# Optimization experiments

Hardware: AMD Instinct MI355X
Metric: run time of the kernel (lower is better)

The kernel has to match this reference:

```python
import jax, jax.numpy as jnp
import numpy as np

N, D, DB, E, H = 1024, 512, 64, 32768, 1024

def setup_inputs() -> dict:
    key = jax.random.key(0)
    k = jax.random.split(key, 6)
    object_feats = jax.random.normal(k[0], (N, D), dtype=jnp.float32)
    bboxes_embedding = jax.random.normal(k[1], (N, N, DB), dtype=jnp.float32)
    pairs = jax.random.randint(k[2], (E, 2), 0, N, dtype=jnp.int64)
    # Kaiming-normal-ish init for the two Linear layers
    W1 = jax.random.normal(k[3], (D + D + DB, H), dtype=jnp.float32) * np.sqrt(2.0 / (D + D + DB))
    b1 = jnp.zeros((H,), dtype=jnp.float32)
    W2 = jax.random.normal(k[4], (H, D), dtype=jnp.float32) * np.sqrt(2.0 / H)
    b2 = jnp.zeros((D,), dtype=jnp.float32)
    return {"object_feats": object_feats, "bboxes_embedding": bboxes_embedding,
            "pairs": pairs, "W1": W1, "b1": b1, "W2": W2, "b2": b2}

def reference(object_feats, bboxes_embedding, pairs, W1, b1, W2, b2):
    sub = pairs[:, 0]
    obj = pairs[:, 1]
    # gather pair features: [E, D] each, plus pairwise bbox embedding [E, DB]
    f_sub = object_feats[sub]
    f_obj = object_feats[obj]
    bb = bboxes_embedding[sub, obj]
    x = jnp.concatenate((f_sub, f_obj, bb), axis=1)  # [E, 2D+DB]
    h = jax.nn.relu(x @ W1 + b1)
    out = h @ W2 + b2  # [E, D]
    n = object_feats.shape[0]
    # scatter-mean into subject nodes; each node's own feature is included once,
    # so new_feat[i] = (object_feats[i] + sum_{pairs with sub==i} out) / (1 + count[i]).
    # Nodes with no incident pairs keep their original feature (count==0 -> identity).
    seg_sum = jax.ops.segment_sum(out, sub, num_segments=n)  # [N, D]
    count = jax.ops.segment_sum(jnp.ones((out.shape[0],), dtype=out.dtype), sub, num_segments=n)
    new_feats = (object_feats + seg_sum) / (1.0 + count)[:, None]
    return (new_feats, bboxes_embedding, pairs)
```

## Files before the change

### kernel.cpp

```cpp
#include <hip/hip_runtime.h>

#define N_OBJ 1024
#define E_P   32768

typedef float f32x4 __attribute__((ext_vector_type(4)));
typedef short bf16x8 __attribute__((ext_vector_type(8)));
typedef unsigned short u16x4 __attribute__((ext_vector_type(4)));

__device__ __forceinline__ unsigned short f2bf(float f) {
    unsigned u = __float_as_uint(f);
    u = u + 0x7FFFu + ((u >> 16) & 1u);
    return (unsigned short)(u >> 16);
}

#define CP_OFF_PREP 0
#define CP_LEN_PREP 2097152
#define CP_OFF_PRE  (CP_OFF_PREP + CP_LEN_PREP)
#define CP_LEN_PRE  1048576
#define CP_OFF_PQ   (CP_OFF_PRE + CP_LEN_PRE)
#define CP_LEN_PQ   3145728
#define CP_OFF_SEG  (CP_OFF_PQ + CP_LEN_PQ)
#define CP_LEN_SEG  5242880
#define CP_OFF_OUT  (CP_OFF_SEG + CP_LEN_SEG)
#define CP_LEN_OUT  5242880

__device__ __forceinline__ void copy_role(const float4* __restrict__ src,
                                          float4* __restrict__ dst,
                                          int off, int len, int nblocks, int cb) {
    int i = off + cb * 256 + threadIdx.x;
    int end = off + len;
    int stride = nblocks * 256;
    for (; i < end; i += stride) dst[i] = src[i];
}

__global__ __launch_bounds__(256) void k_prep(const float* __restrict__ W1,
                                              const float* __restrict__ W2,
                                              const float* __restrict__ feats,
                                              unsigned short* __restrict__ w1pqT,
                                              unsigned short* __restrict__ w1cT,
                                              unsigned short* __restrict__ w2T,
                                              unsigned short* __restrict__ featsb,
                                              const float4* __restrict__ csrc,
                                              float4* __restrict__ cdst) {
    int bid = blockIdx.x;
    if ((bid % 3) == 2) { copy_role(csrc, cdst, CP_OFF_PREP, CP_LEN_PREP, 928, bid / 3); return; }
    int job = (bid / 3) * 2 + (bid % 3);
    int tid = threadIdx.x;
    if (job >= 1600) {
        int base = (job - 1600) * 2048 + tid * 8;
        float4 v0 = *(const float4*)&feats[base];
        float4 v1 = *(const float4*)&feats[base + 4];
        u16x4 o0 = { f2bf(v0.x), f2bf(v0.y), f2bf(v0.z), f2bf(v0.w) };
        u16x4 o1 = { f2bf(v1.x), f2bf(v1.y), f2bf(v1.z), f2bf(v1.w) };
        *(u16x4*)&featsb[base] = o0;
        *(u16x4*)&featsb[base + 4] = o1;
        return;
    }
    const float* in; unsigned short* out;
    int LDI, LDO, r0, c0, nbase, kbase;
    if (job < 1024) {
        int t = job; r0 = (t >> 5) * 32; c0 = (t & 31) * 32;
        in = W1; LDI = 1024; out = w1pqT; LDO = 512;
        nbase = c0 + (r0 >= 512 ? 1024 : 0); kbase = r0 & 511;
    } else if (job < 1088) {
        int t = job - 1024; r0 = 1024 + (t >> 5) * 32; c0 = (t & 31) * 32;
        in = W1; LDI = 1024; out = w1cT; LDO = 64;
        nbase = c0; kbase = r0 - 1024;
    } else {
        int t = job - 1088; r0 = (t >> 4) * 32; c0 = (t & 15) * 32;
        in = W2; LDI = 512; out = w2T; LDO = 1024;
        nbase = c0; kbase = r0;
    }
    __shared__ float lds[32][33];
    int ti = tid >> 3, tj = (tid & 7) * 4;
    float4 v = *(const float4*)&in[(size_t)(r0 + ti) * LDI + c0 + tj];
    lds[ti][tj] = v.x; lds[ti][tj + 1] = v.y; lds[ti][tj + 2] = v.z; lds[ti][tj + 3] = v.w;
    __syncthreads();
    int oc = tid >> 3, oj = (tid & 7) * 4;
    u16x4 o = { f2bf(lds[oj][oc]), f2bf(lds[oj + 1][oc]), f2bf(lds[oj + 2][oc]), f2bf(lds[oj + 3][oc]) };
    *(u16x4*)&out[(size_t)(nbase + oc) * LDO + kbase + oj] = o;
}

__global__ __launch_bounds__(256) void k_pre(const int* __restrict__ pairs,
                                             float* __restrict__ out_pairs,
                                             int* __restrict__ counts,
                                             const float4* __restrict__ csrc,
                                             float4* __restrict__ cdst) {
    int bid = blockIdx.x;
    if ((bid % 3) < 2) { copy_role(csrc, cdst, CP_OFF_PRE, CP_LEN_PRE, 512, (bid / 3) * 2 + (bid % 3)); return; }
    int i = (bid / 3) * 256 + threadIdx.x;
    if (i < 2 * E_P) out_pairs[i] = (float)pairs[i];
    if (i < E_P) atomicAdd(&counts[pairs[2 * i]], 1);
}

__global__ __launch_bounds__(256) void k_scan(const int* __restrict__ counts,
                                              int* __restrict__ offsets,
                                              int* __restrict__ cursor,
                                              int* __restrict__ brec,
                                              int* __restrict__ bcnt) {
    __shared__ int buf[2][256];
    int tid = threadIdx.x;
    int c[4]; int s = 0;
    #pragma unroll
    for (int i = 0; i < 4; ++i) { c[i] = counts[tid * 4 + i]; s += c[i]; }
    buf[0][tid] = s;
    __syncthreads();
    int sel = 0;
    for (int d = 1; d < 256; d <<= 1) {
        int v = buf[sel][tid];
        if (tid >= d) v += buf[sel][tid - d];
        buf[sel ^ 1][tid] = v;
        sel ^= 1;
        __syncthreads();
    }
    int base = buf[sel][tid] - s;
    int run = base;
    #pragma unroll
    for (int i = 0; i < 4; ++i) {
        offsets[tid * 4 + i] = run;
        cursor[tid * 4 + i]  = run;
        run += c[i];
    }
    if (tid == 255) offsets[1024] = run;
    int nb[4]; int t = 0;
    #pragma unroll
    for (int i = 0; i < 4; ++i) { nb[i] = (c[i] + 15) >> 4; t += nb[i]; }
    __syncthreads();
    buf[0][tid] = t;
    __syncthreads();
    sel = 0;
    for (int d = 1; d < 256; d <<= 1) {
        int v = buf[sel][tid];
        if (tid >= d) v += buf[sel][tid - d];
        buf[sel ^ 1][tid] = v;
        sel ^= 1;
        __syncthreads();
    }
    int bpos = buf[sel][tid] - t;
    #pragma unroll
    for (int i = 0; i < 4; ++i) {
        int seg = tid * 4 + i;
        for (int k = 0; k < nb[i]; ++k) brec[bpos++] = (seg << 8) | k;
    }
    if (tid == 255) bcnt[0] = bpos;
}

__global__ __launch_bounds__(256) void k_pq(const unsigned short* __restrict__ featsb,
                                            const unsigned short* __restrict__ w1pqT,
                                            const float* __restrict__ b1,
                                            float* __restrict__ P, float* __restrict__ Q,
                                            const int* __restrict__ pairs,
                                            int* __restrict__ cursor,
                                            int* __restrict__ csr,
                                            const float4* __restrict__ csrc,
                                            float4* __restrict__ cdst) {
    int bid = blockIdx.x;
    if (bid >= 1536) {
        int e = (bid - 1536) * 256 + threadIdx.x;
        if (e < E_P) {
            int sidx = pairs[2 * e];
            int pos = atomicAdd(&cursor[sidx], 1);
            csr[pos] = e;
        }
        return;
    }
    if ((bid % 3) < 2) { copy_role(csrc, cdst, CP_OFF_PQ, CP_LEN_PQ, 1024, (bid / 3) * 2 + (bid % 3)); return; }
    int job = bid / 3;
    int m0 = (job >> 5) * 64, n0 = (job & 31) * 64;
    int tid = threadIdx.x, w = tid >> 6, l = tid & 63;
    int ln = l & 15, kb = (l >> 4) * 8;
    int row = m0 + w * 16 + ln;
    f32x4 acc[4] = {};
    for (int k0 = 0; k0 < 512; k0 += 32) {
        bf16x8 a = *(const bf16x8*)&featsb[(size_t)row * 512 + k0 + kb];
        #pragma unroll
        for (int f = 0; f < 4; ++f) {
            bf16x8 b = *(const bf16x8*)&w1pqT[(size_t)(n0 + f * 16 + ln) * 512 + k0 + kb];
            acc[f] = __builtin_amdgcn_mfma_f32_16x16x32_bf16(a, b, acc[f], 0, 0, 0);
        }
    }
    int mr = m0 + w * 16 + (l >> 4) * 4;
    if (n0 < 1024) {
        #pragma unroll
        for (int f = 0; f < 4; ++f) {
            int n = n0 + f * 16 + ln;
            float b1v = b1[n];
            #pragma unroll
            for (int r = 0; r < 4; ++r)
                P[(size_t)(mr + r) * 1024 + n] = acc[f][r] + b1v;
        }
    } else {
        #pragma unroll
        for (int f = 0; f < 4; ++f) {
            int n = n0 - 1024 + f * 16 + ln;
            #pragma unroll
            for (int r = 0; r < 4; ++r)
                Q[(size_t)(mr + r) * 1024 + n] = acc[f][r];
        }
    }
}

__global__ __launch_bounds__(256) void k_seg(const int* __restrict__ csr,
                                             const int* __restrict__ offsets,
                                             const int* __restrict__ brec,
                                             const int* __restrict__ bcnt,
                                             const int* __restrict__ pairs,
                                             const float* __restrict__ bb,
                                             const unsigned short* __restrict__ w1cT,
                                             const float* __restrict__ P,
                                             const float* __restrict__ Q,
                                             float* __restrict__ HS,
                                             const float4* __restrict__ csrc,
                                             float4* __restrict__ cdst) {
    int bid = blockIdx.x;
    if ((bid % 3) == 0) { copy_role(csrc, cdst, CP_OFF_SEG, CP_LEN_SEG, 1536, bid / 3); return; }
    int b = (bid / 3) * 2 + (bid % 3) - 1;
    if (b >= bcnt[0]) return;
    int rec = brec[b];
    int seg = rec >> 8, kchunk = rec & 255;
    int start = offsets[seg] + kchunk * 16;
    int end = offsets[seg + 1];
    int n = end - start; if (n > 16) n = 16;

    const int tid = threadIdx.x, w = tid >> 6, l = tid & 63;
    const int ln = l & 15, g = l >> 4, kb = g * 8;
    const int n0 = w * 256;

    int idx = start + ln; int last = end - 1; if (idx > last) idx = last;
    int e = csr[idx];
    int obj = pairs[2 * e + 1];
    const float* br = &bb[((size_t)seg * 1024 + (size_t)obj) * 64];
    float4 a0 = *(const float4*)&br[kb];
    float4 a1 = *(const float4*)&br[kb + 4];
    float4 a2 = *(const float4*)&br[32 + kb];
    float4 a3 = *(const float4*)&br[32 + kb + 4];
    bf16x8 A0, A1;
    A0[0] = (short)f2bf(a0.x); A0[1] = (short)f2bf(a0.y); A0[2] = (short)f2bf(a0.z); A0[3] = (short)f2bf(a0.w);
    A0[4] = (short)f2bf(a1.x); A0[5] = (short)f2bf(a1.y); A0[6] = (short)f2bf(a1.z); A0[7] = (short)f2bf(a1.w);
    A1[0] = (short)f2bf(a2.x); A1[1] = (short)f2bf(a2.y); A1[2] = (short)f2bf(a2.z); A1[3] = (short)f2bf(a2.w);
    A1[4] = (short)f2bf(a3.x); A1[5] = (short)f2bf(a3.y); A1[6] = (short)f2bf(a3.z); A1[7] = (short)f2bf(a3.w);

    int ra0 = __shfl(obj, g * 4 + 0);
    int ra1 = __shfl(obj, g * 4 + 1);
    int ra2 = __shfl(obj, g * 4 + 2);
    int ra3 = __shfl(obj, g * 4 + 3);
    bool v0 = (g * 4 + 0) < n;
    bool v1 = (g * 4 + 1) < n;
    bool v2 = (g * 4 + 2) < n;
    bool v3 = (g * 4 + 3) < n;

    float pv[16];
    #pragma unroll
    for (int f = 0; f < 16; ++f)
        pv[f] = P[(size_t)seg * 1024 + n0 + f * 16 + ln];

    #pragma unroll
    for (int f = 0; f < 16; ++f) {
        const unsigned short* wr = &w1cT[(size_t)(n0 + f * 16 + ln) * 64];
        bf16x8 b0 = *(const bf16x8*)&wr[kb];
        bf16x8 b1v = *(const bf16x8*)&wr[32 + kb];
        f32x4 d = {0.f, 0.f, 0.f, 0.f};
        d = __builtin_amdgcn_mfma_f32_16x16x32_bf16(A0, b0, d, 0, 0, 0);
        d = __builtin_amdgcn_mfma_f32_16x16x32_bf16(A1, b1v, d, 0, 0, 0);
        int col = n0 + f * 16 + ln;
        float q0 = Q[(size_t)ra0 * 1024 + col];
        float q1 = Q[(size_t)ra1 * 1024 + col];
        float q2 = Q[(size_t)ra2 * 1024 + col];
        float q3 = Q[(size_t)ra3 * 1024 + col];
        float h = 0.f;
        h += v0 ? fmaxf(d[0] + pv[f] + q0, 0.f) : 0.f;
        h += v1 ? fmaxf(d[1] + pv[f] + q1, 0.f) : 0.f;
        h += v2 ? fmaxf(d[2] + pv[f] + q2, 0.f) : 0.f;
        h += v3 ? fmaxf(d[3] + pv[f] + q3, 0.f) : 0.f;
        h += __shfl_xor(h, 16);
        h += __shfl_xor(h, 32);
        if (l < 16) atomicAdd(&HS[(size_t)seg * 1024 + n0 + f * 16 + l], h);
    }
}

__global__ __launch_bounds__(256) void k_out(const float* __restrict__ HS,
                                             const unsigned short* __restrict__ w2T,
                                             const float* __restrict__ feats,
                                             const float* __restrict__ b2,
                                             const int* __restrict__ counts,
                                             float* __restrict__ out0,
                                             const float4* __restrict__ csrc,
                                             float4* __restrict__ cdst) {
    int bid = blockIdx.x;
    if ((bid % 13) != 12) { copy_role(csrc, cdst, CP_OFF_OUT, CP_LEN_OUT, 1536, (bid / 13) * 12 + (bid % 13)); return; }
    int job = bid / 13;
    int m0 = (job >> 3) * 64, n0 = (job & 7) * 64;
    int tid = threadIdx.x, w = tid >> 6, l = tid & 63;
    int ln = l & 15, kb = (l >> 4) * 8;
    int row = m0 + w * 16 + ln;
    f32x4 acc[4] = {};
    for (int k0 = 0; k0 < 1024; k0 += 32) {
        const float* hp = &HS[(size_t)row * 1024 + k0 + kb];
        float4 h0 = *(const float4*)&hp[0];
        float4 h1 = *(const float4*)&hp[4];
        bf16x8 a;
        a[0] = (short)f2bf(h0.x); a[1] = (short)f2bf(h0.y); a[2] = (short)f2bf(h0.z); a[3] = (short)f2bf(h0.w);
        a[4] = (short)f2bf(h1.x); a[5] = (short)f2bf(h1.y); a[6] = (short)f2bf(h1.z); a[7] = (short)f2bf(h1.w);
        #pragma unroll
        for (int f = 0; f < 4; ++f) {
            bf16x8 b = *(const bf16x8*)&w2T[(size_t)(n0 + f * 16 + ln) * 1024 + k0 + kb];
            acc[f] = __builtin_amdgcn_mfma_f32_16x16x32_bf16(a, b, acc[f], 0, 0, 0);
        }
    }
    int mr = m0 + w * 16 + (l >> 4) * 4;
    float cv[4], inv[4];
    #pragma unroll
    for (int r = 0; r < 4; ++r) {
        float c = (float)counts[mr + r];
        cv[r] = c;
        inv[r] = 1.0f / (1.0f + c);
    }
    #pragma unroll
    for (int f = 0; f < 4; ++f) {
        int n = n0 + f * 16 + ln;
        float b2v = b2[n];
        #pragma unroll
        for (int r = 0; r < 4; ++r) {
            float fv = feats[(size_t)(mr + r) * 512 + n];
            out0[(size_t)(mr + r) * 512 + n] = (fv + acc[f][r] + cv[r] * b2v) * inv[r];
        }
    }
}

extern "C" void kernel_launch(void* const* d_in, const int* in_sizes, int n_in,
                              void* d_out, int out_size, void* d_ws, size_t ws_size,
                              hipStream_t stream) {
    const float* feats = (const float*)d_in[0];
    const float* bb    = (const float*)d_in[1];
    const int*   pairs = (const int*)d_in[2];
    const float* W1    = (const float*)d_in[3];
    const float* b1    = (const float*)d_in[4];
    const float* W2    = (const float*)d_in[5];
    const float* b2    = (const float*)d_in[6];

    float* out        = (float*)d_out;
    float* out_feats  = out;
    float* out_bb     = out + (size_t)N_OBJ * 512;
    float* out_pairs  = out + (size_t)N_OBJ * 512 + (size_t)N_OBJ * N_OBJ * 64;

    char* w = (char*)d_ws;
    unsigned short* featsb = (unsigned short*)w;
    unsigned short* w1pqT  = (unsigned short*)(w + (1u << 20));
    float*          HS     = (float*)w;
    unsigned short* w1cT   = (unsigned short*)(w + (4u << 20));
    unsigned short* w2T    = (unsigned short*)(w + (4u << 20) + (128u << 10));
    float* P = (float*)(w + (5u << 20) + (128u << 10));
    float* Q = (float*)(w + (9u << 20) + (128u << 10));
    char* ints = w + (13u << 20) + (128u << 10);
    int* counts  = (int*)ints;
    int* offsets = (int*)(ints + 4096);
    int* cursor  = (int*)(ints + 12288);
    int* csr     = (int*)(ints + 16384);
    int* brec    = (int*)(ints + 16384 + 131072);
    int* bcnt    = (int*)(ints + 16384 + 131072 + 16384);

    const float4* cbb  = (const float4*)bb;
    float4*       cobb = (float4*)out_bb;

    hipMemsetAsync(counts, 0, 4096, stream);

    k_prep<<<2784, 256, 0, stream>>>(W1, W2, feats, w1pqT, w1cT, w2T, featsb, cbb, cobb);
    k_pre<<<768, 256, 0, stream>>>(pairs, out_pairs, counts, cbb, cobb);
    k_scan<<<1, 256, 0, stream>>>(counts, offsets, cursor, brec, bcnt);
    k_pq<<<1664, 256, 0, stream>>>(featsb, w1pqT, b1, P, Q, pairs, cursor, csr, cbb, cobb);

    hipMemsetAsync(HS, 0, (size_t)N_OBJ * 1024 * sizeof(float), stream);

    k_seg<<<4608, 256, 0, stream>>>(csr, offsets, brec, bcnt, pairs, bb, w1cT, P, Q, HS, cbb, cobb);
    k_out<<<1664, 256, 0, stream>>>(HS, w2T, feats, b2, counts, out_feats, cbb, cobb);
}
```

Baseline: 248.1 us.

## Merge prep kernels, pack CSR records, process 32 pairs per segment block

Merges k_prep and k_pre into one kernel, and gives the scan kernel extra blocks that do part of the bbox copy. The CSR now stores object indices directly, and block records pack start, segment and count, so k_seg avoids the offsets and pairs lookups. Each k_seg block now handles up to 32 pairs as two MFMA groups that share the weight loads and the HS atomics, which halves the number of atomics and blocks. The copy work is rebalanced across kernels and the copy loop is unrolled by two, at the cost of higher register pressure in k_seg.

```diff
diff --git a/kernel.cpp b/kernel.cpp
--- a/kernel.cpp
+++ b/kernel.cpp
@@ -13,39 +13,53 @@
     return (unsigned short)(u >> 16);
 }
 
-#define CP_OFF_PREP 0
-#define CP_LEN_PREP 2097152
-#define CP_OFF_PRE  (CP_OFF_PREP + CP_LEN_PREP)
-#define CP_LEN_PRE  1048576
-#define CP_OFF_PQ   (CP_OFF_PRE + CP_LEN_PRE)
-#define CP_LEN_PQ   3145728
-#define CP_OFF_SEG  (CP_OFF_PQ + CP_LEN_PQ)
-#define CP_LEN_SEG  5242880
-#define CP_OFF_OUT  (CP_OFF_SEG + CP_LEN_SEG)
-#define CP_LEN_OUT  5242880
+#define OFF_A    0
+#define LEN_A    2097152
+#define OFF_SCAN (OFF_A + LEN_A)
+#define LEN_SCAN 1048576
+#define OFF_PQ   (OFF_SCAN + LEN_SCAN)
+#define LEN_PQ   3145728
+#define OFF_SEG  (OFF_PQ + LEN_PQ)
+#define LEN_SEG  7340032
+#define OFF_OUT  (OFF_SEG + LEN_SEG)
+#define LEN_OUT  3145728
 
 __device__ __forceinline__ void copy_role(const float4* __restrict__ src,
                                           float4* __restrict__ dst,
-                                          int off, int len, int nblocks, int cb) {
+                                          int off, int len, int nb, int cb) {
+    int stride = nb * 256;
     int i = off + cb * 256 + threadIdx.x;
     int end = off + len;
-    int stride = nblocks * 256;
-    for (; i < end; i += stride) dst[i] = src[i];
-}
-
-__global__ __launch_bounds__(256) void k_prep(const float* __restrict__ W1,
-                                              const float* __restrict__ W2,
-                                              const float* __restrict__ feats,
-                                              unsigned short* __restrict__ w1pqT,
-                                              unsigned short* __restrict__ w1cT,
-                                              unsigned short* __restrict__ w2T,
-                                              unsigned short* __restrict__ featsb,
-                                              const float4* __restrict__ csrc,
-                                              float4* __restrict__ cdst) {
-    int bid = blockIdx.x;
-    if ((bid % 3) == 2) { copy_role(csrc, cdst, CP_OFF_PREP, CP_LEN_PREP, 928, bid / 3); return; }
+    for (; i + stride < end; i += 2 * stride) {
+        float4 a = src[i];
+        float4 b = src[i + stride];
+        dst[i] = a;
+        dst[i + stride] = b;
+    }
+    if (i < end) dst[i] = src[i];
+}
+
+__global__ __launch_bounds__(256) void k_a(const float* __restrict__ W1,
+                                           const float* __restrict__ W2,
+                                           const float* __restrict__ feats,
+                                           const int* __restrict__ pairs,
+                                           unsigned short* __restrict__ w1pqT,
+                                           unsigned short* __restrict__ w1cT,
+                                           unsigned short* __restrict__ w2T,
+                                           unsigned short* __restrict__ featsb,
+                                           float* __restrict__ out_pairs,
+                                           int* __restrict__ counts,
+                                           const float4* __restrict__ csrc,
+                                           float4* __restrict__ cdst) {
+    int bid = blockIdx.x, tid = threadIdx.x;
+    if ((bid % 3) == 2) { copy_role(csrc, cdst, OFF_A, LEN_A, 1056, bid / 3); return; }
     int job = (bid / 3) * 2 + (bid % 3);
-    int tid = threadIdx.x;
+    if (job >= 1856) {
+        int i = (job - 1856) * 256 + tid;
+        out_pairs[i] = (float)pairs[i];
+        if (i < E_P) atomicAdd(&counts[pairs[2 * i]], 1);
+        return;
+    }
     if (job >= 1600) {
         int base = (job - 1600) * 2048 + tid * 8;
         float4 v0 = *(const float4*)&feats[base];
@@ -59,7 +73,7 @@
     const float* in; unsigned short* out;
     int LDI, LDO, r0, c0, nbase, kbase;
     if (job < 1024) {
-        int t = job; r0 = (t >> 5) * 32; c0 = (t & 31) * 32;
+        r0 = (job >> 5) * 32; c0 = (job & 31) * 32;
         in = W1; LDI = 1024; out = w1pqT; LDO = 512;
         nbase = c0 + (r0 >= 512 ? 1024 : 0); kbase = r0 & 511;
     } else if (job < 1088) {
@@ -77,29 +91,20 @@
     lds[ti][tj] = v.x; lds[ti][tj + 1] = v.y; lds[ti][tj + 2] = v.z; lds[ti][tj + 3] = v.w;
     __syncthreads();
     int oc = tid >> 3, oj = (tid & 7) * 4;
-    u16x4 o = { f2bf(lds[oj][oc]), f2bf(lds[oj + 1][oc]), f2bf(lds[oj + 2][oc]), f2bf(lds[oj + 3][oc]) };
+    u16x4 o = { f2bf(lds[oj][oc]), f2bf(lds[oj + 1][oc]),
+                f2bf(lds[oj + 2][oc]), f2bf(lds[oj + 3][oc]) };
     *(u16x4*)&out[(size_t)(nbase + oc) * LDO + kbase + oj] = o;
 }
 
-__global__ __launch_bounds__(256) void k_pre(const int* __restrict__ pairs,
-                                             float* __restrict__ out_pairs,
-                                             int* __restrict__ counts,
-                                             const float4* __restrict__ csrc,
-                                             float4* __restrict__ cdst) {
-    int bid = blockIdx.x;
-    if ((bid % 3) < 2) { copy_role(csrc, cdst, CP_OFF_PRE, CP_LEN_PRE, 512, (bid / 3) * 2 + (bid % 3)); return; }
-    int i = (bid / 3) * 256 + threadIdx.x;
-    if (i < 2 * E_P) out_pairs[i] = (float)pairs[i];
-    if (i < E_P) atomicAdd(&counts[pairs[2 * i]], 1);
-}
-
 __global__ __launch_bounds__(256) void k_scan(const int* __restrict__ counts,
-                                              int* __restrict__ offsets,
                                               int* __restrict__ cursor,
-                                              int* __restrict__ brec,
-                                              int* __restrict__ bcnt) {
+                                              unsigned* __restrict__ brec,
+                                              int* __restrict__ bcnt,
+                                              const float4* __restrict__ csrc,
+                                              float4* __restrict__ cdst) {
+    int bid = blockIdx.x, tid = threadIdx.x;
+    if (bid != 0) { copy_role(csrc, cdst, OFF_SCAN, LEN_SCAN, 1024, bid - 1); return; }
     __shared__ int buf[2][256];
-    int tid = threadIdx.x;
     int c[4]; int s = 0;
     #pragma unroll
     for (int i = 0; i < 4; ++i) { c[i] = counts[tid * 4 + i]; s += c[i]; }
@@ -116,15 +121,10 @@
     int base = buf[sel][tid] - s;
     int run = base;
     #pragma unroll
-    for (int i = 0; i < 4; ++i) {
-        offsets[tid * 4 + i] = run;
-        cursor[tid * 4 + i]  = run;
-        run += c[i];
-    }
-    if (tid == 255) offsets[1024] = run;
+    for (int i = 0; i < 4; ++i) { cursor[tid * 4 + i] = run; run += c[i]; }
     int nb[4]; int t = 0;
     #pragma unroll
-    for (int i = 0; i < 4; ++i) { nb[i] = (c[i] + 15) >> 4; t += nb[i]; }
+    for (int i = 0; i < 4; ++i) { nb[i] = (c[i] + 31) >> 5; t += nb[i]; }
     __syncthreads();
     buf[0][tid] = t;
     __syncthreads();
@@ -137,10 +137,16 @@
         __syncthreads();
     }
     int bpos = buf[sel][tid] - t;
+    int run2 = base;
     #pragma unroll
     for (int i = 0; i < 4; ++i) {
         int seg = tid * 4 + i;
-        for (int k = 0; k < nb[i]; ++k) brec[bpos++] = (seg << 8) | k;
+        for (int k = 0; k < nb[i]; ++k) {
+            int st = run2 + k * 32;
+            int cnt = c[i] - k * 32; if (cnt > 32) cnt = 32;
+            brec[bpos++] = (unsigned)st | ((unsigned)seg << 16) | ((unsigned)(cnt - 1) << 26);
+        }
+        run2 += c[i];
     }
     if (tid == 255) bcnt[0] = bpos;
 }
@@ -151,20 +157,18 @@
                                             float* __restrict__ P, float* __restrict__ Q,
                                             const int* __restrict__ pairs,
                                             int* __restrict__ cursor,
-                                            int* __restrict__ csr,
+                                            int* __restrict__ csr_obj,
                                             const float4* __restrict__ csrc,
                                             float4* __restrict__ cdst) {
     int bid = blockIdx.x;
     if (bid >= 1536) {
         int e = (bid - 1536) * 256 + threadIdx.x;
-        if (e < E_P) {
-            int sidx = pairs[2 * e];
-            int pos = atomicAdd(&cursor[sidx], 1);
-            csr[pos] = e;
-        }
+        int sidx = pairs[2 * e];
+        int pos = atomicAdd(&cursor[sidx], 1);
+        csr_obj[pos] = pairs[2 * e + 1];
         return;
     }
-    if ((bid % 3) < 2) { copy_role(csrc, cdst, CP_OFF_PQ, CP_LEN_PQ, 1024, (bid / 3) * 2 + (bid % 3)); return; }
+    if ((bid % 3) < 2) { copy_role(csrc, cdst, OFF_PQ, LEN_PQ, 1024, (bid / 3) * 2 + (bid % 3)); return; }
     int job = bid / 3;
     int m0 = (job >> 5) * 64, n0 = (job & 31) * 64;
     int tid = threadIdx.x, w = tid >> 6, l = tid & 63;
@@ -200,11 +204,9 @@
     }
 }
 
-__global__ __launch_bounds__(256) void k_seg(const int* __restrict__ csr,
-                                             const int* __restrict__ offsets,
-                                             const int* __restrict__ brec,
+__global__ __launch_bounds__(256) void k_seg(const int* __restrict__ csr_obj,
+                                             const unsigned* __restrict__ brec,
                                              const int* __restrict__ bcnt,
-                                             const int* __restrict__ pairs,
                                              const float* __restrict__ bb,
                                              const unsigned short* __restrict__ w1cT,
                                              const float* __restrict__ P,
@@ -213,65 +215,84 @@
                                              const float4* __restrict__ csrc,
                                              float4* __restrict__ cdst) {
     int bid = blockIdx.x;
-    if ((bid % 3) == 0) { copy_role(csrc, cdst, CP_OFF_SEG, CP_LEN_SEG, 1536, bid / 3); return; }
-    int b = (bid / 3) * 2 + (bid % 3) - 1;
+    if ((bid % 2) == 0) { copy_role(csrc, cdst, OFF_SEG, LEN_SEG, 2048, bid / 2); return; }
+    int b = bid / 2;
     if (b >= bcnt[0]) return;
-    int rec = brec[b];
-    int seg = rec >> 8, kchunk = rec & 255;
-    int start = offsets[seg] + kchunk * 16;
-    int end = offsets[seg + 1];
-    int n = end - start; if (n > 16) n = 16;
+    unsigned rec = brec[b];
+    const int start = rec & 0xFFFF;
+    const int seg = (rec >> 16) & 0x3FF;
+    const int n = ((rec >> 26) & 31) + 1;
 
     const int tid = threadIdx.x, w = tid >> 6, l = tid & 63;
-    const int ln = l & 15, g = l >> 4, kb = g * 8;
+    const int ln = l & 15, g4 = l >> 4, kb = g4 * 8;
     const int n0 = w * 256;
-
-    int idx = start + ln; int last = end - 1; if (idx > last) idx = last;
-    int e = csr[idx];
-    int obj = pairs[2 * e + 1];
-    const float* br = &bb[((size_t)seg * 1024 + (size_t)obj) * 64];
-    float4 a0 = *(const float4*)&br[kb];
-    float4 a1 = *(const float4*)&br[kb + 4];
-    float4 a2 = *(const float4*)&br[32 + kb];
-    float4 a3 = *(const float4*)&br[32 + kb + 4];
-    bf16x8 A0, A1;
-    A0[0] = (short)f2bf(a0.x); A0[1] = (short)f2bf(a0.y); A0[2] = (short)f2bf(a0.z); A0[3] = (short)f2bf(a0.w);
-    A0[4] = (short)f2bf(a1.x); A0[5] = (short)f2bf(a1.y); A0[6] = (short)f2bf(a1.z); A0[7] = (short)f2bf(a1.w);
-    A1[0] = (short)f2bf(a2.x); A1[1] = (short)f2bf(a2.y); A1[2] = (short)f2bf(a2.z); A1[3] = (short)f2bf(a2.w);
-    A1[4] = (short)f2bf(a3.x); A1[5] = (short)f2bf(a3.y); A1[6] = (short)f2bf(a3.z); A1[7] = (short)f2bf(a3.w);
-
-    int ra0 = __shfl(obj, g * 4 + 0);
-    int ra1 = __shfl(obj, g * 4 + 1);
-    int ra2 = __shfl(obj, g * 4 + 2);
-    int ra3 = __shfl(obj, g * 4 + 3);
-    bool v0 = (g * 4 + 0) < n;
-    bool v1 = (g * 4 + 1) < n;
-    bool v2 = (g * 4 + 2) < n;
-    bool v3 = (g * 4 + 3) < n;
-
-    float pv[16];
-    #pragma unroll
-    for (int f = 0; f < 16; ++f)
-        pv[f] = P[(size_t)seg * 1024 + n0 + f * 16 + ln];
-
-    #pragma unroll
+    const int nA = n < 16 ? n : 16;
+    const int nB = n - 16;
+
+    int iA = start + (ln < nA ? ln : nA - 1);
+    int iB = (nB > 0) ? (start + 16 + (ln < nB ? ln : nB - 1)) : iA;
+    int objA = csr_obj[iA];
+    int objB = csr_obj[iB];
+
+    const float* brA = &bb[((size_t)seg * 1024 + (size_t)objA) * 64];
+    const float* brB = &bb[((size_t)seg * 1024 + (size_t)objB) * 64];
+    float4 a0 = *(const float4*)&brA[kb];
+    float4 a1 = *(const float4*)&brA[kb + 4];
+    float4 a2 = *(const float4*)&brA[32 + kb];
+    float4 a3 = *(const float4*)&brA[32 + kb + 4];
+    float4 c0 = *(const float4*)&brB[kb];
+    float4 c1 = *(const float4*)&brB[kb + 4];
+    float4 c2 = *(const float4*)&brB[32 + kb];
+    float4 c3 = *(const float4*)&brB[32 + kb + 4];
+    bf16x8 A0a, A1a, A0b, A1b;
+    A0a[0] = (short)f2bf(a0.x); A0a[1] = (short)f2bf(a0.y); A0a[2] = (short)f2bf(a0.z); A0a[3] = (short)f2bf(a0.w);
+    A0a[4] = (short)f2bf(a1.x); A0a[5] = (short)f2bf(a1.y); A0a[6] = (short)f2bf(a1.z); A0a[7] = (short)f2bf(a1.w);
+    A1a[0] = (short)f2bf(a2.x); A1a[1] = (short)f2bf(a2.y); A1a[2] = (short)f2bf(a2.z); A1a[3] = (short)f2bf(a2.w);
+    A1a[4] = (short)f2bf(a3.x); A1a[5] = (short)f2bf(a3.y); A1a[6] = (short)f2bf(a3.z); A1a[7] = (short)f2bf(a3.w);
+    A0b[0] = (short)f2bf(c0.x); A0b[1] = (short)f2bf(c0.y); A0b[2] = (short)f2bf(c0.z); A0b[3] = (short)f2bf(c0.w);
+    A0b[4] = (short)f2bf(c1.x); A0b[5] = (short)f2bf(c1.y); A0b[6] = (short)f2bf(c1.z); A0b[7] = (short)f2bf(c1.w);
+    A1b[0] = (short)f2bf(c2.x); A1b[1] = (short)f2bf(c2.y); A1b[2] = (short)f2bf(c2.z); A1b[3] = (short)f2bf(c2.w);
+    A1b[4] = (short)f2bf(c3.x); A1b[5] = (short)f2bf(c3.y); A1b[6] = (short)f2bf(c3.z); A1b[7] = (short)f2bf(c3.w);
+
+    int raA0 = __shfl(objA, g4 * 4 + 0), raA1 = __shfl(objA, g4 * 4 + 1);
+    int raA2 = __shfl(objA, g4 * 4 + 2), raA3 = __shfl(objA, g4 * 4 + 3);
+    int raB0 = __shfl(objB, g4 * 4 + 0), raB1 = __shfl(objB, g4 * 4 + 1);
+    int raB2 = __shfl(objB, g4 * 4 + 2), raB3 = __shfl(objB, g4 * 4 + 3);
+    bool vA0 = (g4 * 4 + 0) < nA, vA1 = (g4 * 4 + 1) < nA;
+    bool vA2 = (g4 * 4 + 2) < nA, vA3 = (g4 * 4 + 3) < nA;
+    bool vB0 = (g4 * 4 + 0) < nB, vB1 = (g4 * 4 + 1) < nB;
+    bool vB2 = (g4 * 4 + 2) < nB, vB3 = (g4 * 4 + 3) < nB;
+
+    #pragma unroll 4
     for (int f = 0; f < 16; ++f) {
-        const unsigned short* wr = &w1cT[(size_t)(n0 + f * 16 + ln) * 64];
+        int col = n0 + f * 16 + ln;
+        const unsigned short* wr = &w1cT[(size_t)col * 64];
         bf16x8 b0 = *(const bf16x8*)&wr[kb];
-        bf16x8 b1v = *(const bf16x8*)&wr[32 + kb];
-        f32x4 d = {0.f, 0.f, 0.f, 0.f};
-        d = __builtin_amdgcn_mfma_f32_16x16x32_bf16(A0, b0, d, 0, 0, 0);
-        d = __builtin_amdgcn_mfma_f32_16x16x32_bf16(A1, b1v, d, 0, 0, 0);
-        int col = n0 + f * 16 + ln;
-        float q0 = Q[(size_t)ra0 * 1024 + col];
-        float q1 = Q[(size_t)ra1 * 1024 + col];
-        float q2 = Q[(size_t)ra2 * 1024 + col];
-        float q3 = Q[(size_t)ra3 * 1024 + col];
+        bf16x8 b1 = *(const bf16x8*)&wr[32 + kb];
+        f32x4 dA = {0.f, 0.f, 0.f, 0.f};
+        dA = __builtin_amdgcn_mfma_f32_16x16x32_bf16(A0a, b0, dA, 0, 0, 0);
+        dA = __builtin_amdgcn_mfma_f32_16x16x32_bf16(A1a, b1, dA, 0, 0, 0);
+        f32x4 dB = {0.f, 0.f, 0.f, 0.f};
+        dB = __builtin_amdgcn_mfma_f32_16x16x32_bf16(A0b, b0, dB, 0, 0, 0);
+        dB = __builtin_amdgcn_mfma_f32_16x16x32_bf16(A1b, b1, dB, 0, 0, 0);
+        float pv = P[(size_t)seg * 1024 + col];
+        float qA0 = Q[(size_t)raA0 * 1024 + col];
+        float qA1 = Q[(size_t)raA1 * 1024 + col];
+        float qA2 = Q[(size_t)raA2 * 1024 + col];
+        float qA3 = Q[(size_t)raA3 * 1024 + col];
+        float qB0 = Q[(size_t)raB0 * 1024 + col];
+        float qB1 = Q[(size_t)raB1 * 1024 + col];
+        float qB2 = Q[(size_t)raB2 * 1024 + col];
+        float qB3 = Q[(size_t)raB3 * 1024 + col];
         float h = 0.f;
-        h += v0 ? fmaxf(d[0] + pv[f] + q0, 0.f) : 0.f;
-        h += v1 ? fmaxf(d[1] + pv[f] + q1, 0.f) : 0.f;
-        h += v2 ? fmaxf(d[2] + pv[f] + q2, 0.f) : 0.f;
-        h += v3 ? fmaxf(d[3] + pv[f] + q3, 0.f) : 0.f;
+        h += vA0 ? fmaxf(dA[0] + pv + qA0, 0.f) : 0.f;
+        h += vA1 ? fmaxf(dA[1] + pv + qA1, 0.f) : 0.f;
+        h += vA2 ? fmaxf(dA[2] + pv + qA2, 0.f) : 0.f;
+        h += vA3 ? fmaxf(dA[3] + pv + qA3, 0.f) : 0.f;
+        h += vB0 ? fmaxf(dB[0] + pv + qB0, 0.f) : 0.f;
+        h += vB1 ? fmaxf(dB[1] + pv + qB1, 0.f) : 0.f;
+        h += vB2 ? fmaxf(dB[2] + pv + qB2, 0.f) : 0.f;
+        h += vB3 ? fmaxf(dB[3] + pv + qB3, 0.f) : 0.f;
         h += __shfl_xor(h, 16);
         h += __shfl_xor(h, 32);
         if (l < 16) atomicAdd(&HS[(size_t)seg * 1024 + n0 + f * 16 + l], h);
@@ -287,8 +308,8 @@
                                              const float4* __restrict__ csrc,
                                              float4* __restrict__ cdst) {
     int bid = blockIdx.x;
-    if ((bid % 13) != 12) { copy_role(csrc, cdst, CP_OFF_OUT, CP_LEN_OUT, 1536, (bid / 13) * 12 + (bid % 13)); return; }
-    int job = bid / 13;
+    if ((bid % 9) != 8) { copy_role(csrc, cdst, OFF_OUT, LEN_OUT, 1024, (bid / 9) * 8 + (bid % 9)); return; }
+    int job = bid / 9;
     int m0 = (job >> 3) * 64, n0 = (job & 7) * 64;
     int tid = threadIdx.x, w = tid >> 6, l = tid & 63;
     int ln = l & 15, kb = (l >> 4) * 8;
@@ -352,25 +373,24 @@
     float* P = (float*)(w + (5u << 20) + (128u << 10));
     float* Q = (float*)(w + (9u << 20) + (128u << 10));
     char* ints = w + (13u << 20) + (128u << 10);
-    int* counts  = (int*)ints;
-    int* offsets = (int*)(ints + 4096);
-    int* cursor  = (int*)(ints + 12288);
-    int* csr     = (int*)(ints + 16384);
-    int* brec    = (int*)(ints + 16384 + 131072);
-    int* bcnt    = (int*)(ints + 16384 + 131072 + 16384);
+    int*      counts  = (int*)ints;
+    int*      cursor  = (int*)(ints + 4096);
+    int*      csr_obj = (int*)(ints + 8192);
+    unsigned* brec    = (unsigned*)(ints + 8192 + 131072);
+    int*      bcnt    = (int*)(ints + 8192 + 131072 + 16384);
 
     const float4* cbb  = (const float4*)bb;
     float4*       cobb = (float4*)out_bb;
 
     hipMemsetAsync(counts, 0, 4096, stream);
 
-    k_prep<<<2784, 256, 0, stream>>>(W1, W2, feats, w1pqT, w1cT, w2T, featsb, cbb, cobb);
-    k_pre<<<768, 256, 0, stream>>>(pairs, out_pairs, counts, cbb, cobb);
-    k_scan<<<1, 256, 0, stream>>>(counts, offsets, cursor, brec, bcnt);
-    k_pq<<<1664, 256, 0, stream>>>(featsb, w1pqT, b1, P, Q, pairs, cursor, csr, cbb, cobb);
+    k_a<<<3168, 256, 0, stream>>>(W1, W2, feats, pairs, w1pqT, w1cT, w2T, featsb,
+                                  out_pairs, counts, cbb, cobb);
+    k_scan<<<1025, 256, 0, stream>>>(counts, cursor, brec, bcnt, cbb, cobb);
+    k_pq<<<1664, 256, 0, stream>>>(featsb, w1pqT, b1, P, Q, pairs, cursor, csr_obj, cbb, cobb);
 
     hipMemsetAsync(HS, 0, (size_t)N_OBJ * 1024 * sizeof(float), stream);
 
-    k_seg<<<4608, 256, 0, stream>>>(csr, offsets, brec, bcnt, pairs, bb, w1cT, P, Q, HS, cbb, cobb);
-    k_out<<<1664, 256, 0, stream>>>(HS, w2T, feats, b2, counts, out_feats, cbb, cobb);
-}
+    k_seg<<<4096, 256, 0, stream>>>(csr_obj, brec, bcnt, bb, w1cT, P, Q, HS, cbb, cobb);
+    k_out<<<1152, 256, 0, stream>>>(HS, w2T, feats, b2, counts, out_feats, cbb, cobb);
+}
```

After: 230.5 us. 7.1% less time.
